# Performance work log

Measured on AMD Instinct MI355X. Metric: run time of the kernel, lower is better.

The kernel has to match this reference:

```python
import jax, jax.numpy as jnp
import numpy as np
from jax import lax

ANCHOR_AREAS = (128.0**2, 256.0**2, 512.0**2)
ASPECT_RATIOS = (0.5, 1.0, 2.0)
STRIDE = 32.0                      # resnet backbone: get_orig_stat maps fm -> input via x*32
PRE_NMS_TOP_N = 2000
POST_NMS_TOP_N = 100
NMS_IOU_T = 0.7
SCORE_T = 0.1
MIN_SCALE = 0.01
BBOX_XFORM_CLIP = float(np.log(1000.0 / 16.0))


def make_anchors(H, W):
    # anchors laid out in (H, W, A) order to match the offset permutation below
    sizes = []
    for area in ANCHOR_AREAS:
        for r in ASPECT_RATIOS:          # aspect_ratio = w / h
            sizes.append((np.sqrt(area * r), np.sqrt(area / r)))
    sizes = jnp.asarray(np.asarray(sizes, dtype=np.float32))  # [A, 2] (w, h)
    cy = (jnp.arange(H, dtype=jnp.float32) + 0.5) * STRIDE
    cx = (jnp.arange(W, dtype=jnp.float32) + 0.5) * STRIDE
    cyg, cxg = jnp.meshgrid(cy, cx, indexing='ij')             # [H, W]
    cxg = cxg[:, :, None]
    cyg = cyg[:, :, None]
    w = sizes[:, 0]
    h = sizes[:, 1]
    anchors = jnp.stack([cxg - w / 2, cyg - h / 2, cxg + w / 2, cyg + h / 2], axis=-1)
    return anchors.reshape(-1, 4)                              # [H*W*A, 4] xyxy


def decode_boxes(anchors, offsets):
    # anchors [N,4], offsets [B,N,4] (tx, ty, tw, th) -> boxes [B,N,4] xyxy
    wa = anchors[:, 2] - anchors[:, 0]
    ha = anchors[:, 3] - anchors[:, 1]
    cxa = anchors[:, 0] + 0.5 * wa
    cya = anchors[:, 1] + 0.5 * ha
    tx, ty = offsets[..., 0], offsets[..., 1]
    tw = jnp.minimum(offsets[..., 2], BBOX_XFORM_CLIP)
    th = jnp.minimum(offsets[..., 3], BBOX_XFORM_CLIP)
    px = tx * wa + cxa
    py = ty * ha + cya
    pw = jnp.exp(tw) * wa
    ph = jnp.exp(th) * ha
    return jnp.stack([px - pw / 2, py - ph / 2, px + pw / 2, py + ph / 2], axis=-1)


def box_iou(a, b):
    area_a = (a[:, 2] - a[:, 0]) * (a[:, 3] - a[:, 1])
    area_b = (b[:, 2] - b[:, 0]) * (b[:, 3] - b[:, 1])
    lt = jnp.maximum(a[:, None, :2], b[None, :, :2])
    rb = jnp.minimum(a[:, None, 2:], b[None, :, 2:])
    wh = jnp.clip(rb - lt, 0.0)
    inter = wh[..., 0] * wh[..., 1]
    return inter / (area_a[:, None] + area_b[None, :] - inter + 1e-9)


def nms_single(boxes, scores):
    # boxes [P,4] sorted by descending score; invalid entries carry score -1
    P = boxes.shape[0]
    iou = box_iou(boxes, boxes)
    idx = jnp.arange(P)

    def body(i, keep):
        sup = (iou[i] > NMS_IOU_T) & (idx > i)
        return jnp.where(keep[i], keep & (~sup), keep)

    keep = lax.stop_gradient(lax.fori_loop(0, P, body, scores > 0.0))
    kept_scores = jnp.where(keep, scores, -1.0)
    top_s, top_i = lax.top_k(kept_scores, POST_NMS_TOP_N)
    return boxes[top_i], top_s


def rpn_forward(features, W1, b1, W2, b2, W3, b3):
    B, Cin, H, W = features.shape
    A = W3.shape[0]
    # 3x3 sliding conv + ReLU
    t = lax.conv_general_dilated(
        features, W1, window_strides=(1, 1), padding='SAME',
        dimension_numbers=('NCHW', 'OIHW', 'NCHW'))
    t = jax.nn.relu(t + b1[None, :, None, None])
    # 1x1 sibling heads as channel contractions
    offs = jnp.einsum('bchw,oc->bohw', t, W2) + b2[None, :, None, None]   # [B, A*4, H, W]
    logits = jnp.einsum('bchw,oc->bohw', t, W3) + b3[None, :, None, None]  # [B, A, H, W]
    # reorder to per-anchor layout (H, W, A)
    offs = offs.reshape(B, A, 4, H, W).transpose(0, 3, 4, 1, 2).reshape(B, -1, 4)
    scores = jax.nn.sigmoid(logits.transpose(0, 2, 3, 1).reshape(B, -1))  # [B, N]
    anchors = make_anchors(H, W)
    boxes = decode_boxes(anchors, offs)                                    # [B, N, 4]
    # clip to image boundary (handle_cross_boundary_boxes during testing)
    img_w, img_h = W * STRIDE, H * STRIDE
    boxes = jnp.stack([
        jnp.clip(boxes[..., 0], 0.0, img_w),
        jnp.clip(boxes[..., 1], 0.0, img_h),
        jnp.clip(boxes[..., 2], 0.0, img_w),
        jnp.clip(boxes[..., 3], 0.0, img_h)], axis=-1)
    # score-threshold + min-scale filtering
    bw = boxes[..., 2] - boxes[..., 0]
    bh = boxes[..., 3] - boxes[..., 1]
    valid = (scores >= SCORE_T) & (bw > MIN_SCALE * img_w) & (bh > MIN_SCALE * img_h)
    masked = jnp.where(valid, scores, -1.0)
    # pre-NMS top-k, then per-image NMS + post-NMS top-n
    top_s, top_i = lax.top_k(masked, PRE_NMS_TOP_N)                        # [B, P]
    top_boxes = jnp.take_along_axis(boxes, top_i[..., None], axis=1)       # [B, P, 4]
    out_boxes, out_scores = jax.vmap(nms_single)(top_boxes, top_s)
    return out_boxes, out_scores                                           # [B,100,4], [B,100]


def setup_inputs() -> dict:
    key = jax.random.key(0)
    ks = jax.random.split(key, 4)
    B, Cin, H, W = 8, 1024, 50, 50
    A = 9
    C = 512
    return {
        'features': jax.random.normal(ks[0], (B, Cin, H, W), jnp.float32),
        'W1': jax.random.normal(ks[1], (C, Cin, 3, 3), jnp.float32) * 0.01,
        'b1': jnp.zeros((C,), jnp.float32),
        'W2': jax.random.normal(ks[2], (A * 4, C), jnp.float32) * 0.01,
        'b2': jnp.zeros((A * 4,), jnp.float32),
        'W3': jax.random.normal(ks[3], (A, C), jnp.float32) * 0.01,
        'b3': jnp.zeros((A,), jnp.float32),
    }


def reference(features, W1, b1, W2, b2, W3, b3):
    return rpn_forward(features, W1, b1, W2, b2, W3, b3)
```

## Files before the change

### kernel.cpp

```cpp
#include <hip/hip_runtime.h>
#include <cstdint>

#define NB 8
#define CIN 1024
#define HDIM 50
#define WDIM 50
#define COUT 512
#define NA 9
#define NANCH (HDIM*WDIM*NA)
#define PRE_N 2000
#define POST_N 100

typedef __attribute__((ext_vector_type(8))) short bf16x8;
typedef __attribute__((ext_vector_type(4))) float f32x4;
typedef __attribute__((ext_vector_type(16))) float f32x16;
typedef __attribute__((ext_vector_type(8))) unsigned short ushort8v;

constexpr size_t TPLANE    = 20578304;
constexpr size_t OFF_TPH   = 0;
constexpr size_t OFF_TPL   = 20578304;
constexpr size_t OFF_BOXES = 41156608;
constexpr size_t OFF_KEYS  = 44036608;
constexpr size_t OFF_TBOX  = 45476608;
constexpr size_t OFF_TS    = 45732608;
constexpr size_t OFF_SUP   = 45796608;
constexpr size_t QDIM      = 2976;
constexpr size_t PLSTRIDE  = QDIM * 8;
constexpr size_t PPLANE    = 48758784;
constexpr size_t OFF_PH    = 49892864;
constexpr size_t OFF_PL    = OFF_PH + PPLANE;
constexpr size_t WPLANE    = 9437184;
constexpr size_t OFF_WH    = 147410432;
constexpr size_t OFF_WL    = OFF_WH + WPLANE;

__device__ __forceinline__ void split2bf16(float v, unsigned short &hi, unsigned short &lo) {
    unsigned int u = __float_as_uint(v);
    unsigned int r = u + 0x7FFFu + ((u >> 16) & 1u);
    hi = (unsigned short)(r >> 16);
    float hf = __uint_as_float(((unsigned int)hi) << 16);
    float lf = v - hf;
    unsigned int u2 = __float_as_uint(lf);
    unsigned int r2 = u2 + 0x7FFFu + ((u2 >> 16) & 1u);
    lo = (unsigned short)(r2 >> 16);
}

__device__ __forceinline__ void gl_lds(const unsigned short* g, unsigned short* l) {
    __builtin_amdgcn_global_load_lds(
        (const __attribute__((address_space(1))) unsigned int*)(const void*)g,
        (__attribute__((address_space(3))) unsigned int*)(void*)l,
        16, 0, 0);
}

__global__ __launch_bounds__(256) void prep_all(const float* __restrict__ f,
                                                const float* __restrict__ W1,
                                                unsigned short* __restrict__ Ph,
                                                unsigned short* __restrict__ Pl,
                                                unsigned short* __restrict__ Wh,
                                                unsigned short* __restrict__ Wl) {
    int blk = blockIdx.x;
    if (blk < 5952) {
        int id = blk * 256 + threadIdx.x;
        int q = id % (int)QDIM; int r = id / (int)QDIM;
        int cic = r % 64; int b = r / 64;
        int pp = q - 53;
        int rr = pp / 52, cc = pp - rr * 52;
        int h = rr - 1, w = cc - 1;
        bool inb = (pp >= 0) && (pp < 2704) && (h >= 0) && (h < HDIM) && (w >= 0) && (w < WDIM);
        ushort8v hv0, lv0, hv1, lv1;
#pragma unroll
        for (int j = 0; j < 16; ++j) {
            float v = 0.f;
            if (inb) v = f[(((size_t)b * CIN + cic * 16 + j) * HDIM + h) * WDIM + w];
            unsigned short hi, lo;
            split2bf16(v, hi, lo);
            if (j < 8) { hv0[j] = hi; lv0[j] = lo; }
            else       { hv1[j - 8] = hi; lv1[j - 8] = lo; }
        }
        size_t b0 = ((size_t)((b * 64 + cic) * 2 + 0)) * PLSTRIDE + (size_t)q * 8;
        size_t b1 = ((size_t)((b * 64 + cic) * 2 + 1)) * PLSTRIDE + (size_t)q * 8;
        *(ushort8v*)&Ph[b0] = hv0;
        *(ushort8v*)&Ph[b1] = hv1;
        *(ushort8v*)&Pl[b0] = lv0;
        *(ushort8v*)&Pl[b1] = lv1;
    } else {
        int id = (blk - 5952) * 256 + threadIdx.x;
        int co = id % 64; int r = id / 64;
        int cic = r % 64; int cot = r / 64;
        int cog = cot * 64 + co;
        const float* src = W1 + ((size_t)cog * CIN + cic * 16) * 9;
        float v[144];
#pragma unroll
        for (int i = 0; i < 36; ++i) {
            float4 x = ((const float4*)src)[i];
            v[i * 4 + 0] = x.x; v[i * 4 + 1] = x.y; v[i * 4 + 2] = x.z; v[i * 4 + 3] = x.w;
        }
#pragma unroll
        for (int tap = 0; tap < 9; ++tap) {
            ushort8v hv0, lv0, hv1, lv1;
#pragma unroll
            for (int j = 0; j < 16; ++j) {
                unsigned short hi, lo;
                split2bf16(v[j * 9 + tap], hi, lo);
                if (j < 8) { hv0[j] = hi; lv0[j] = lo; }
                else       { hv1[j - 8] = hi; lv1[j - 8] = lo; }
            }
            size_t base = (((size_t)(cot * 64 + cic) * 9 + tap) * 2) * 512;
            *(ushort8v*)&Wh[base + co * 8]       = hv0;
            *(ushort8v*)&Wh[base + 512 + co * 8] = hv1;
            *(ushort8v*)&Wl[base + co * 8]       = lv0;
            *(ushort8v*)&Wl[base + 512 + co * 8] = lv1;
        }
    }
}

__global__ __launch_bounds__(256, 1) void conv_mfma(const unsigned short* __restrict__ FPh,
                                                    const unsigned short* __restrict__ FPl,
                                                    const unsigned short* __restrict__ WPh,
                                                    const unsigned short* __restrict__ WPl,
                                                    const float* __restrict__ b1,
                                                    unsigned short* __restrict__ Tph,
                                                    unsigned short* __restrict__ Tpl) {
    extern __shared__ unsigned short smem[];

    int blk = blockIdx.x;
    int logical = (blk & 7) * 88 + (blk >> 3);
    int cot = logical & 7;
    int ptile = (logical >> 3) % 11;
    int b = logical / 88;
    int co0 = cot * 64;
    int P0 = 32 + ptile * 256;

    int t = threadIdx.x, wv = t >> 6, ln = t & 63;
    int lm = ln & 31, lk = ln >> 5;

    f32x16 acc[2][2];
#pragma unroll
    for (int jm = 0; jm < 2; ++jm)
#pragma unroll
        for (int jn = 0; jn < 2; ++jn)
#pragma unroll
            for (int rg = 0; rg < 16; ++rg) acc[jm][jn][rg] = 0.f;

    auto stage = [&](int cur, int cic) {
        unsigned short* bA = smem + cur * 30720;
        unsigned short* bB = bA + 12288;
#pragma unroll
        for (int k = 0; k < 15; ++k) {
            int id = wv * 15 + k;
            if (id < 24) {
                int hl = id / 12, lkc = (id / 6) & 1, s = id % 6;
                const unsigned short* pl = hl ? FPl : FPh;
                const unsigned short* src = pl
                    + ((size_t)((b * 64 + cic) * 2 + lkc)) * PLSTRIDE
                    + (size_t)P0 * 8 + s * 512 + ln * 8;
                gl_lds(src, &bA[(hl * 2 + lkc) * 3072 + s * 512]);
            } else {
                int j = id - 24;
                int hl = j / 18, s = j % 18;
                const unsigned short* pl = hl ? WPl : WPh;
                const unsigned short* src = pl + (size_t)(cot * 64 + cic) * 9216 + s * 512 + ln * 8;
                gl_lds(src, &bB[hl * 9216 + s * 512]);
            }
        }
    };

    auto compute = [&](int cur) {
        const unsigned short* bA = smem + cur * 30720;
        const unsigned short* bB = bA + 12288;
#pragma unroll
        for (int tap = 0; tap < 9; ++tap) {
            const int kh = tap / 3, kw = tap % 3;
            const int dlt = (kh - 1) * 52 + (kw - 1);
            bf16x8 a[2][2], bb[2][2];
#pragma unroll
            for (int jm = 0; jm < 2; ++jm) {
                int e = (wv * 2 + jm) * 32 + lm + dlt + 53;
                int ad = e * 8;
                a[jm][0] = *(const bf16x8*)&bA[(0 * 2 + lk) * 3072 + ad];
                a[jm][1] = *(const bf16x8*)&bA[(1 * 2 + lk) * 3072 + ad];
            }
#pragma unroll
            for (int jn = 0; jn < 2; ++jn) {
                int bd = tap * 1024 + lk * 512 + (jn * 32 + lm) * 8;
                bb[jn][0] = *(const bf16x8*)&bB[0 * 9216 + bd];
                bb[jn][1] = *(const bf16x8*)&bB[1 * 9216 + bd];
            }
#pragma unroll
            for (int jm = 0; jm < 2; ++jm)
#pragma unroll
                for (int jn = 0; jn < 2; ++jn) {
                    acc[jm][jn] = __builtin_amdgcn_mfma_f32_32x32x16_bf16(a[jm][0], bb[jn][0], acc[jm][jn], 0, 0, 0);
                    acc[jm][jn] = __builtin_amdgcn_mfma_f32_32x32x16_bf16(a[jm][0], bb[jn][1], acc[jm][jn], 0, 0, 0);
                    acc[jm][jn] = __builtin_amdgcn_mfma_f32_32x32x16_bf16(a[jm][1], bb[jn][0], acc[jm][jn], 0, 0, 0);
                }
        }
    };

    stage(0, 0);
    __syncthreads();

#pragma unroll 1
    for (int cc = 0; cc < 32; ++cc) {
        stage(1, 2 * cc + 1);
        compute(0);
        __syncthreads();
        if (cc < 31) stage(0, 2 * cc + 2);
        compute(1);
        __syncthreads();
    }

#pragma unroll
    for (int jn = 0; jn < 2; ++jn) {
        int co = co0 + jn * 32 + lm;
        float bv = b1[co];
#pragma unroll
        for (int jm = 0; jm < 2; ++jm) {
#pragma unroll
            for (int rg = 0; rg < 16; ++rg) {
                int mrow = (rg & 3) + 8 * (rg >> 2) + 4 * lk;
                int pp = P0 + (wv * 2 + jm) * 32 + mrow;
                int rr = pp / 52, cc = pp - rr * 52;
                int h = rr - 1, w = cc - 1;
                if ((unsigned)h < HDIM && (unsigned)w < WDIM) {
                    float v = fmaxf(acc[jm][jn][rg] + bv, 0.f);
                    unsigned short hi, lo;
                    split2bf16(v, hi, lo);
                    int px = b * 2500 + h * 50 + w;
                    size_t sa = (((((size_t)(px >> 7) * 16 + (co >> 5)) * 8 + ((px >> 4) & 7)) * 4
                                  + ((co >> 3) & 3)) * 16 + (px & 15)) * 8 + (co & 7);
                    Tph[sa] = hi;
                    Tpl[sa] = lo;
                }
            }
        }
    }
}

__global__ __launch_bounds__(256) void proj_decode_mfma(const unsigned short* __restrict__ Tph,
                                                        const unsigned short* __restrict__ Tpl,
                                                        const float* __restrict__ W2,
                                                        const float* __restrict__ b2,
                                                        const float* __restrict__ W3,
                                                        const float* __restrict__ b3,
                                                        float* __restrict__ boxes,
                                                        unsigned long long* __restrict__ keys) {
    __shared__ unsigned short sTh[4096], sTl[4096];
    __shared__ unsigned short sWh[1536], sWl[1536];
    __shared__ float pout[128 * 46];

    int blk = blockIdx.x;
    int px0 = blk * 128;
    int t = threadIdx.x, wv = t >> 6, ln = t & 63;
    int lm = ln & 15, q = ln >> 4;

    f32x4 acc[2][3];
#pragma unroll
    for (int jm = 0; jm < 2; ++jm)
#pragma unroll
        for (int nf = 0; nf < 3; ++nf) acc[jm][nf] = (f32x4){0.f, 0.f, 0.f, 0.f};

#pragma unroll 1
    for (int cc16 = 0; cc16 < 16; ++cc16) {
        __syncthreads();
        size_t base = ((size_t)blk * 16 + cc16) * 4096;
        if (wv == 0) {
#pragma unroll
            for (int s = 0; s < 4; ++s) gl_lds(Tph + base + s * 512 + ln * 8, &sTh[s * 512]);
        } else if (wv == 1) {
#pragma unroll
            for (int s = 4; s < 8; ++s) gl_lds(Tph + base + s * 512 + ln * 8, &sTh[s * 512]);
        } else if (wv == 2) {
#pragma unroll
            for (int s = 0; s < 4; ++s) gl_lds(Tpl + base + s * 512 + ln * 8, &sTl[s * 512]);
        } else {
#pragma unroll
            for (int s = 4; s < 8; ++s) gl_lds(Tpl + base + s * 512 + ln * 8, &sTl[s * 512]);
        }
        int c0 = cc16 * 32;
        for (int idx = t; idx < 1536; idx += 256) {
            int o = idx >> 5, ci = idx & 31;
            float v = 0.f;
            if (o < 36) v = W2[o * 512 + c0 + ci];
            else if (o < 45) v = W3[(o - 36) * 512 + c0 + ci];
            unsigned short hi, lo;
            split2bf16(v, hi, lo);
            int ad = (((o >> 4) * 4 + (ci >> 3)) * 16 + (o & 15)) * 8 + (ci & 7);
            sWh[ad] = hi; sWl[ad] = lo;
        }
        __syncthreads();

        bf16x8 a[2][2], bb[3][2];
#pragma unroll
        for (int jm = 0; jm < 2; ++jm) {
            int mf = wv * 2 + jm;
            int ad = ((mf * 4 + q) * 16 + lm) * 8;
            a[jm][0] = *(const bf16x8*)&sTh[ad];
            a[jm][1] = *(const bf16x8*)&sTl[ad];
        }
#pragma unroll
        for (int nf = 0; nf < 3; ++nf) {
            int ad = ((nf * 4 + q) * 16 + lm) * 8;
            bb[nf][0] = *(const bf16x8*)&sWh[ad];
            bb[nf][1] = *(const bf16x8*)&sWl[ad];
        }
#pragma unroll
        for (int jm = 0; jm < 2; ++jm)
#pragma unroll
            for (int nf = 0; nf < 3; ++nf) {
                acc[jm][nf] = __builtin_amdgcn_mfma_f32_16x16x32_bf16(a[jm][0], bb[nf][0], acc[jm][nf], 0, 0, 0);
                acc[jm][nf] = __builtin_amdgcn_mfma_f32_16x16x32_bf16(a[jm][0], bb[nf][1], acc[jm][nf], 0, 0, 0);
                acc[jm][nf] = __builtin_amdgcn_mfma_f32_16x16x32_bf16(a[jm][1], bb[nf][0], acc[jm][nf], 0, 0, 0);
            }
    }
    __syncthreads();
#pragma unroll
    for (int jm = 0; jm < 2; ++jm)
#pragma unroll
        for (int nf = 0; nf < 3; ++nf) {
            int o = nf * 16 + lm;
            if (o < 45) {
                float bias = (o < 36) ? b2[o] : b3[o - 36];
#pragma unroll
                for (int rg = 0; rg < 4; ++rg) {
                    int pxl = (wv * 2 + jm) * 16 + q * 4 + rg;
                    pout[pxl * 46 + o] = acc[jm][nf][rg] + bias;
                }
            }
        }
    __syncthreads();

    const float AW[9] = {90.50966799187809f, 128.0f, 181.01933598375618f,
                         181.01933598375618f, 256.0f, 362.03867196751236f,
                         362.03867196751236f, 512.0f, 724.0773439350247f};
    const float AH[9] = {181.01933598375618f, 128.0f, 90.50966799187809f,
                         362.03867196751236f, 256.0f, 181.01933598375618f,
                         724.0773439350247f, 512.0f, 362.03867196751236f};
    const float CLIPV = 4.135166556742356f;
    const float IMG = 1600.0f;

    for (int it = t; it < 128 * 9; it += 256) {
        int pxl = it / 9, a = it - pxl * 9;
        int pxg = px0 + pxl;
        if (pxg >= 20000) continue;
        int b = pxg / 2500, rem = pxg % 2500;
        int h = rem / 50, w = rem % 50;

        float tx = pout[pxl * 46 + a * 4 + 0];
        float ty = pout[pxl * 46 + a * 4 + 1];
        float tw = pout[pxl * 46 + a * 4 + 2];
        float th = pout[pxl * 46 + a * 4 + 3];
        float lg = pout[pxl * 46 + 36 + a];

        float s = 1.0f / (1.0f + expf(-lg));

        float cx = ((float)w + 0.5f) * 32.0f;
        float cy = ((float)h + 0.5f) * 32.0f;
        float x1a = cx - 0.5f * AW[a];
        float x2a = cx + 0.5f * AW[a];
        float y1a = cy - 0.5f * AH[a];
        float y2a = cy + 0.5f * AH[a];
        float waf = x2a - x1a;
        float haf = y2a - y1a;
        float cxa = x1a + 0.5f * waf;
        float cya = y1a + 0.5f * haf;

        float twc = tw < CLIPV ? tw : CLIPV;
        float thc = th < CLIPV ? th : CLIPV;
        float pxc = tx * waf + cxa;
        float pyc = ty * haf + cya;
        float pw  = expf(twc) * waf;
        float ph  = expf(thc) * haf;

        float x1 = pxc - 0.5f * pw;
        float y1 = pyc - 0.5f * ph;
        float x2 = pxc + 0.5f * pw;
        float y2 = pyc + 0.5f * ph;
        x1 = fminf(fmaxf(x1, 0.f), IMG);
        y1 = fminf(fmaxf(y1, 0.f), IMG);
        x2 = fminf(fmaxf(x2, 0.f), IMG);
        y2 = fminf(fmaxf(y2, 0.f), IMG);

        float bw = x2 - x1, bh = y2 - y1;
        bool valid = (s >= 0.1f) && (bw > 16.0f) && (bh > 16.0f);
        float m = valid ? s : -1.0f;

        int idx = (h * WDIM + w) * NA + a;
        size_t gi = (size_t)b * NANCH + idx;
        ((float4*)boxes)[gi] = make_float4(x1, y1, x2, y2);
        unsigned int u = __float_as_uint(m);
        unsigned int k32 = (u & 0x80000000u) ? ~u : (u | 0x80000000u);
        keys[gi] = ((unsigned long long)k32 << 15) | (unsigned long long)(32767 - idx);
    }
}

__global__ __launch_bounds__(1024) void select_sort_kernel(const unsigned long long* __restrict__ keys,
                                                           const float* __restrict__ boxes,
                                                           float* __restrict__ top_boxes,
                                                           float* __restrict__ top_s) {
    int b = blockIdx.x;
    int t = threadIdx.x;
    int wv = t >> 6;
    const unsigned long long* kb = keys + (size_t)b * NANCH;

    __shared__ unsigned int whist[16][256];
    __shared__ unsigned int hist[256];
    __shared__ int s_chosen, s_rnew;
    __shared__ unsigned int s_cnt;
    __shared__ unsigned long long skeys[2048];

    const int widths[6] = {8, 8, 8, 8, 8, 7};
    unsigned long long prefix = 0;
    int bitsdone = 0;
    int r = PRE_N;

    for (int p = 0; p < 6; ++p) {
        int width = widths[p];
        int bins = 1 << width;
        int shift = 47 - bitsdone - width;
        for (int i = t; i < 16 * 256; i += 1024) ((unsigned int*)whist)[i] = 0;
        __syncthreads();
        for (int i = t; i < NANCH; i += 1024) {
            unsigned long long k = kb[i];
            if ((k >> (47 - bitsdone)) == prefix)
                atomicAdd(&whist[wv][(unsigned)((k >> shift) & (unsigned long long)(bins - 1))], 1u);
        }
        __syncthreads();
        if (t < bins) {
            unsigned int s = 0;
#pragma unroll
            for (int w = 0; w < 16; ++w) s += whist[w][t];
            hist[t] = s;
        }
        __syncthreads();
        if (t == 0) {
            int acc = 0, chosen = 0, rnew = 1;
            for (int d = bins - 1; d >= 0; --d) {
                int hv = (int)hist[d];
                if (acc + hv >= r) { chosen = d; rnew = r - acc; break; }
                acc += hv;
            }
            s_chosen = chosen;
            s_rnew = rnew;
        }
        __syncthreads();
        prefix = (prefix << width) | (unsigned long long)s_chosen;
        bitsdone += width;
        r = s_rnew;
        __syncthreads();
    }
    unsigned long long Kst = prefix;

    if (t == 0) s_cnt = 0;
    __syncthreads();
    for (int i = t; i < NANCH; i += 1024) {
        unsigned long long k = kb[i];
        if (k >= Kst) {
            unsigned int p = atomicAdd(&s_cnt, 1u);
            if (p < 2048) skeys[p] = k;
        }
    }
    __syncthreads();
    unsigned int cnt = s_cnt;
    for (int i = t; i < 2048; i += 1024)
        if (i >= (int)cnt) skeys[i] = 0ull;
    for (int k = 2; k <= 2048; k <<= 1) {
        for (int j = k >> 1; j > 0; j >>= 1) {
            __syncthreads();
            for (int i = t; i < 2048; i += 1024) {
                int l = i ^ j;
                if (l > i) {
                    unsigned long long a = skeys[i], c = skeys[l];
                    bool up = ((i & k) == 0);
                    if (up ? (a < c) : (a > c)) { skeys[i] = c; skeys[l] = a; }
                }
            }
        }
    }
    __syncthreads();
    for (int i = t; i < PRE_N; i += 1024) {
        unsigned long long k = skeys[i];
        unsigned int k32 = (unsigned int)(k >> 15);
        float m = (k32 & 0x80000000u) ? __uint_as_float(k32 & 0x7FFFFFFFu)
                                      : __uint_as_float(~k32);
        unsigned int idx = 32767u - (unsigned int)(k & 32767ull);
        size_t gi = (size_t)b * NANCH + idx;
        top_s[b * PRE_N + i] = m;
        ((float4*)top_boxes)[b * PRE_N + i] = ((const float4*)boxes)[gi];
    }
}

__global__ __launch_bounds__(256) void sup_kernel(const float* __restrict__ top_boxes,
                                                  unsigned long long* __restrict__ supm) {
    int blk = blockIdx.x;
    int b = blk / 125;
    int chunk = blk % 125;
    int t = threadIdx.x;

    __shared__ float bx1[PRE_N], by1[PRE_N], bx2[PRE_N], by2[PRE_N];
    for (int i = t; i < PRE_N; i += 256) {
        float4 v = ((const float4*)top_boxes)[b * PRE_N + i];
        bx1[i] = v.x; by1[i] = v.y; bx2[i] = v.z; by2[i] = v.w;
    }
    __syncthreads();

    int wave = t >> 6, lane = t & 63;
    for (int rr = 0; rr < 4; ++rr) {
        int i = chunk * 16 + wave * 4 + rr;
        float ax1 = bx1[i], ay1 = by1[i], ax2 = bx2[i], ay2 = by2[i];
        float aarea = (ax2 - ax1) * (ay2 - ay1);
        for (int jw = 0; jw < 32; ++jw) {
            int j = jw * 64 + lane;
            bool sup = false;
            if (j > i && j < PRE_N) {
                float jx1 = bx1[j], jy1 = by1[j], jx2 = bx2[j], jy2 = by2[j];
                float ix1 = fmaxf(ax1, jx1), iy1 = fmaxf(ay1, jy1);
                float ix2 = fminf(ax2, jx2), iy2 = fminf(ay2, jy2);
                float iw = fmaxf(ix2 - ix1, 0.f);
                float ih = fmaxf(iy2 - iy1, 0.f);
                float inter = iw * ih;
                float barea = (jx2 - jx1) * (jy2 - jy1);
                float iou = inter / (aarea + barea - inter + 1e-9f);
                sup = iou > 0.7f;
            }
            unsigned long long m = __ballot(sup);
            if (lane == 0) supm[((size_t)b * PRE_N + i) * 32 + jw] = m;
        }
    }
}

__global__ __launch_bounds__(256) void nms_fin_kernel(const float* __restrict__ top_s,
                                                      const unsigned long long* __restrict__ supm,
                                                      const float* __restrict__ top_boxes,
                                                      float* __restrict__ out) {
    int b = blockIdx.x;
    int t = threadIdx.x;
    __shared__ unsigned int kw[64];
    __shared__ int wpre[65];

    if (t < 64) {
        int lane = t;
        unsigned int alive = 0;
        for (int q = 0; q < 32; ++q) {
            int i = lane * 32 + q;
            if (i < PRE_N && top_s[b * PRE_N + i] > 0.f) alive |= (1u << q);
        }
        const unsigned long long* sm = supm + (size_t)b * PRE_N * 32;
        const unsigned int* sup32 = (const unsigned int*)sm;

        for (int tt = 0; tt < 32; ++tt) {
            unsigned int alo = __shfl(alive, 2 * tt);
            unsigned int ahi = __shfl(alive, 2 * tt + 1);
            unsigned long long talive = (unsigned long long)alo | ((unsigned long long)ahi << 32);
            int i_row = tt * 64 + lane;
            unsigned long long rm = (i_row < PRE_N) ? sm[(size_t)i_row * 32 + tt] : 0ull;

            unsigned long long kept = 0, rem = talive;
            while (rem) {
                int j = __builtin_ctzll(rem);
                kept |= (1ull << j);
                unsigned long long rmj = __shfl(rm, j);
                rem &= ~rmj;
                rem &= ~(1ull << j);
            }

            unsigned int oracc = 0;
            unsigned long long kk = kept;
            while (kk) {
                int j0 = __builtin_ctzll(kk); kk &= kk - 1;
                int j1 = -1, j2 = -1, j3 = -1;
                if (kk) { j1 = __builtin_ctzll(kk); kk &= kk - 1; }
                if (kk) { j2 = __builtin_ctzll(kk); kk &= kk - 1; }
                if (kk) { j3 = __builtin_ctzll(kk); kk &= kk - 1; }
                unsigned int v0 = sup32[(size_t)(tt * 64 + j0) * 64 + lane];
                unsigned int v1 = (j1 >= 0) ? sup32[(size_t)(tt * 64 + j1) * 64 + lane] : 0u;
                unsigned int v2 = (j2 >= 0) ? sup32[(size_t)(tt * 64 + j2) * 64 + lane] : 0u;
                unsigned int v3 = (j3 >= 0) ? sup32[(size_t)(tt * 64 + j3) * 64 + lane] : 0u;
                oracc |= v0 | v1 | v2 | v3;
            }
            alive &= ~oracc;
            if (lane == 2 * tt)     alive = (unsigned int)kept;
            if (lane == 2 * tt + 1) alive = (unsigned int)(kept >> 32);
        }
        kw[lane] = alive;
    }
    __syncthreads();
    if (t == 0) {
        int run = 0;
        for (int w = 0; w < 64; ++w) { wpre[w] = run; run += __popc(kw[w]); }
        wpre[64] = run;
    }
    __syncthreads();
    int total = wpre[64];
    float* out_boxes  = out;
    float* out_scores = out + NB * POST_N * 4;
    for (int i = t; i < PRE_N; i += 256) {
        unsigned int w = kw[i >> 5];
        bool kept = (w >> (i & 31)) & 1u;
        int rk = wpre[i >> 5] + __popc(w & ((1u << (i & 31)) - 1u));
        int pos = kept ? rk : total + (i - rk);
        if (pos < POST_N) {
            out_scores[b * POST_N + pos] = kept ? top_s[b * PRE_N + i] : -1.0f;
            ((float4*)out_boxes)[b * POST_N + pos] = ((const float4*)top_boxes)[b * PRE_N + i];
        }
    }
}

extern "C" void kernel_launch(void* const* d_in, const int* in_sizes, int n_in,
                              void* d_out, int out_size, void* d_ws, size_t ws_size,
                              hipStream_t stream) {
    const float* features = (const float*)d_in[0];
    const float* W1 = (const float*)d_in[1];
    const float* b1 = (const float*)d_in[2];
    const float* W2 = (const float*)d_in[3];
    const float* b2 = (const float*)d_in[4];
    const float* W3 = (const float*)d_in[5];
    const float* b3 = (const float*)d_in[6];
    float* out = (float*)d_out;
    char* ws = (char*)d_ws;

    unsigned short* Tph = (unsigned short*)(ws + OFF_TPH);
    unsigned short* Tpl = (unsigned short*)(ws + OFF_TPL);
    float* boxes   = (float*)(ws + OFF_BOXES);
    unsigned long long* keys = (unsigned long long*)(ws + OFF_KEYS);
    float* top_boxes = (float*)(ws + OFF_TBOX);
    float* top_s     = (float*)(ws + OFF_TS);
    unsigned long long* supm = (unsigned long long*)(ws + OFF_SUP);
    unsigned short* FPh = (unsigned short*)(ws + OFF_PH);
    unsigned short* FPl = (unsigned short*)(ws + OFF_PL);
    unsigned short* WPh = (unsigned short*)(ws + OFF_WH);
    unsigned short* WPl = (unsigned short*)(ws + OFF_WL);

    static bool conv_attr_set = false;
    if (!conv_attr_set) {
        hipFuncSetAttribute(reinterpret_cast<const void*>(&conv_mfma),
                            hipFuncAttributeMaxDynamicSharedMemorySize, 122880);
        conv_attr_set = true;
    }

    prep_all<<<6080, 256, 0, stream>>>(features, W1, FPh, FPl, WPh, WPl);
    conv_mfma<<<704, 256, 122880, stream>>>(FPh, FPl, WPh, WPl, b1, Tph, Tpl);
    proj_decode_mfma<<<157, 256, 0, stream>>>(Tph, Tpl, W2, b2, W3, b3, boxes, keys);
    select_sort_kernel<<<NB, 1024, 0, stream>>>(keys, boxes, top_boxes, top_s);
    sup_kernel<<<NB * 125, 256, 0, stream>>>(top_boxes, supm);
    nms_fin_kernel<<<NB, 256, 0, stream>>>(top_s, supm, top_boxes, out);
}
```

Measured before the change: 1.124 ms.

## Split conv weight staging per tap row to shrink LDS and allow two blocks/CU

The conv kernel now stages weights in chunks of one kernel row (3 taps) instead of all 9 taps at once, double-buffered separately from the activation tile. This cuts dynamic LDS per block so that two blocks can fit per CU, and the launch bounds are raised to request that. It also interleaves the prefetch of the next activation tile across the three tap-row steps and raises wave priority around the MFMA section. In exchange there are three barriers per input-channel chunk instead of one, and the tighter register budget may cause spills.

```diff
diff --git a/kernel.cpp b/kernel.cpp
--- a/kernel.cpp
+++ b/kernel.cpp
@@ -113,7 +113,7 @@
     }
 }
 
-__global__ __launch_bounds__(256, 1) void conv_mfma(const unsigned short* __restrict__ FPh,
+__global__ __launch_bounds__(256, 2) void conv_mfma(const unsigned short* __restrict__ FPh,
                                                     const unsigned short* __restrict__ FPl,
                                                     const unsigned short* __restrict__ WPh,
                                                     const unsigned short* __restrict__ WPl,
@@ -121,6 +121,8 @@
                                                     unsigned short* __restrict__ Tph,
                                                     unsigned short* __restrict__ Tpl) {
     extern __shared__ unsigned short smem[];
+    unsigned short* const Abase = smem;
+    unsigned short* const Bbase = smem + 24576;
 
     int blk = blockIdx.x;
     int logical = (blk & 7) * 88 + (blk >> 3);
@@ -141,72 +143,78 @@
 #pragma unroll
             for (int rg = 0; rg < 16; ++rg) acc[jm][jn][rg] = 0.f;
 
-    auto stage = [&](int cur, int cic) {
-        unsigned short* bA = smem + cur * 30720;
-        unsigned short* bB = bA + 12288;
-#pragma unroll
-        for (int k = 0; k < 15; ++k) {
-            int id = wv * 15 + k;
-            if (id < 24) {
-                int hl = id / 12, lkc = (id / 6) & 1, s = id % 6;
-                const unsigned short* pl = hl ? FPl : FPh;
-                const unsigned short* src = pl
-                    + ((size_t)((b * 64 + cic) * 2 + lkc)) * PLSTRIDE
-                    + (size_t)P0 * 8 + s * 512 + ln * 8;
-                gl_lds(src, &bA[(hl * 2 + lkc) * 3072 + s * 512]);
-            } else {
-                int j = id - 24;
-                int hl = j / 18, s = j % 18;
-                const unsigned short* pl = hl ? WPl : WPh;
-                const unsigned short* src = pl + (size_t)(cot * 64 + cic) * 9216 + s * 512 + ln * 8;
-                gl_lds(src, &bB[hl * 9216 + s * 512]);
-            }
-        }
+    auto stageA = [&](int buf, int cic, int ac) {
+        int hl = ac / 12, lkc = (ac / 6) & 1, s = ac % 6;
+        const unsigned short* pl = hl ? FPl : FPh;
+        const unsigned short* src = pl
+            + ((size_t)((b * 64 + cic) * 2 + lkc)) * PLSTRIDE
+            + (size_t)P0 * 8 + s * 512 + ln * 8;
+        gl_lds(src, &Abase[buf * 12288 + (hl * 2 + lkc) * 3072 + s * 512]);
     };
-
-    auto compute = [&](int cur) {
-        const unsigned short* bA = smem + cur * 30720;
-        const unsigned short* bB = bA + 12288;
-#pragma unroll
-        for (int tap = 0; tap < 9; ++tap) {
-            const int kh = tap / 3, kw = tap % 3;
-            const int dlt = (kh - 1) * 52 + (kw - 1);
-            bf16x8 a[2][2], bb[2][2];
-#pragma unroll
-            for (int jm = 0; jm < 2; ++jm) {
-                int e = (wv * 2 + jm) * 32 + lm + dlt + 53;
-                int ad = e * 8;
-                a[jm][0] = *(const bf16x8*)&bA[(0 * 2 + lk) * 3072 + ad];
-                a[jm][1] = *(const bf16x8*)&bA[(1 * 2 + lk) * 3072 + ad];
-            }
-#pragma unroll
-            for (int jn = 0; jn < 2; ++jn) {
-                int bd = tap * 1024 + lk * 512 + (jn * 32 + lm) * 8;
-                bb[jn][0] = *(const bf16x8*)&bB[0 * 9216 + bd];
-                bb[jn][1] = *(const bf16x8*)&bB[1 * 9216 + bd];
-            }
-#pragma unroll
-            for (int jm = 0; jm < 2; ++jm)
+    auto stageB = [&](int buf, int cic, int tg, int c) {
+        int hl = c / 6, j = c % 6;
+        const unsigned short* pl = hl ? WPl : WPh;
+        const unsigned short* src = pl + (size_t)(cot * 64 + cic) * 9216
+            + (size_t)(tg * 6 + j) * 512 + ln * 8;
+        gl_lds(src, &Bbase[buf * 6144 + hl * 3072 + j * 512]);
+    };
+
+#pragma unroll
+    for (int k = 0; k < 9; ++k) {
+        int id = wv * 9 + k;
+        if (id < 24) stageA(0, 0, id);
+        else         stageB(0, 0, 0, id - 24);
+    }
+    __syncthreads();
+
+#pragma unroll 1
+    for (int cic = 0; cic < 64; ++cic) {
+        int abuf = cic & 1;
+        bool haveA = (cic + 1 < 64);
+#pragma unroll
+        for (int tg = 0; tg < 3; ++tg) {
+            int bbuf = (cic + tg) & 1;
+            int cicb = (tg == 2) ? cic + 1 : cic;
+            int tgn  = (tg == 2) ? 0 : tg + 1;
+            bool haveB = (cicb < 64);
+#pragma unroll
+            for (int k = 0; k < 5; ++k) {
+                int id = wv * 5 + k;
+                if (id < 12) { if (haveB) stageB(bbuf ^ 1, cicb, tgn, id); }
+                else         { if (haveA) stageA(abuf ^ 1, cic + 1, tg * 8 + (id - 12)); }
+            }
+            const unsigned short* bA = Abase + abuf * 12288;
+            const unsigned short* bB = Bbase + bbuf * 6144;
+            __builtin_amdgcn_s_setprio(1);
+#pragma unroll
+            for (int tl = 0; tl < 3; ++tl) {
+                const int dlt = (tg - 1) * 52 + (tl - 1);
+                bf16x8 a[2][2], bb[2][2];
+#pragma unroll
+                for (int jm = 0; jm < 2; ++jm) {
+                    int e = (wv * 2 + jm) * 32 + lm + dlt + 53;
+                    int ad = e * 8;
+                    a[jm][0] = *(const bf16x8*)&bA[(0 * 2 + lk) * 3072 + ad];
+                    a[jm][1] = *(const bf16x8*)&bA[(1 * 2 + lk) * 3072 + ad];
+                }
 #pragma unroll
                 for (int jn = 0; jn < 2; ++jn) {
-                    acc[jm][jn] = __builtin_amdgcn_mfma_f32_32x32x16_bf16(a[jm][0], bb[jn][0], acc[jm][jn], 0, 0, 0);
-                    acc[jm][jn] = __builtin_amdgcn_mfma_f32_32x32x16_bf16(a[jm][0], bb[jn][1], acc[jm][jn], 0, 0, 0);
-                    acc[jm][jn] = __builtin_amdgcn_mfma_f32_32x32x16_bf16(a[jm][1], bb[jn][0], acc[jm][jn], 0, 0, 0);
+                    int bd = tl * 1024 + lk * 512 + (jn * 32 + lm) * 8;
+                    bb[jn][0] = *(const bf16x8*)&bB[bd];
+                    bb[jn][1] = *(const bf16x8*)&bB[3072 + bd];
                 }
-        }
-    };
-
-    stage(0, 0);
-    __syncthreads();
-
-#pragma unroll 1
-    for (int cc = 0; cc < 32; ++cc) {
-        stage(1, 2 * cc + 1);
-        compute(0);
-        __syncthreads();
-        if (cc < 31) stage(0, 2 * cc + 2);
-        compute(1);
-        __syncthreads();
+#pragma unroll
+                for (int jm = 0; jm < 2; ++jm)
+#pragma unroll
+                    for (int jn = 0; jn < 2; ++jn) {
+                        acc[jm][jn] = __builtin_amdgcn_mfma_f32_32x32x16_bf16(a[jm][0], bb[jn][0], acc[jm][jn], 0, 0, 0);
+                        acc[jm][jn] = __builtin_amdgcn_mfma_f32_32x32x16_bf16(a[jm][0], bb[jn][1], acc[jm][jn], 0, 0, 0);
+                        acc[jm][jn] = __builtin_amdgcn_mfma_f32_32x32x16_bf16(a[jm][1], bb[jn][0], acc[jm][jn], 0, 0, 0);
+                    }
+            }
+            __builtin_amdgcn_s_setprio(0);
+            __syncthreads();
+        }
     }
 
 #pragma unroll
@@ -633,12 +641,12 @@
     static bool conv_attr_set = false;
     if (!conv_attr_set) {
         hipFuncSetAttribute(reinterpret_cast<const void*>(&conv_mfma),
-                            hipFuncAttributeMaxDynamicSharedMemorySize, 122880);
+                            hipFuncAttributeMaxDynamicSharedMemorySize, 73728);
         conv_attr_set = true;
     }
 
     prep_all<<<6080, 256, 0, stream>>>(features, W1, FPh, FPl, WPh, WPl);
-    conv_mfma<<<704, 256, 122880, stream>>>(FPh, FPl, WPh, WPl, b1, Tph, Tpl);
+    conv_mfma<<<704, 256, 73728, stream>>>(FPh, FPl, WPh, WPl, b1, Tph, Tpl);
     proj_decode_mfma<<<157, 256, 0, stream>>>(Tph, Tpl, W2, b2, W3, b3, boxes, keys);
     select_sort_kernel<<<NB, 1024, 0, stream>>>(keys, boxes, top_boxes, top_s);
     sup_kernel<<<NB * 125, 256, 0, stream>>>(top_boxes, supm);
```

After: 1.098 ms. 2.3% less time.
